# Optimization experiments

Measured on AMD Instinct MI355X. Metric: run time of the kernel, lower is better.

The kernel has to match this reference:

```python
import jax, jax.numpy as jnp
import numpy as np

B, S, IN, HID = 16, 4096, 512, 512
NH = 4
HD = HID // NH            # 128
NA = 4 * 2                # num_attractors*2 = 8 codes per head
EPS = 1e-5


def _ln(x, g, b):
    m = jnp.mean(x, axis=-1, keepdims=True)
    v = jnp.mean((x - m) ** 2, axis=-1, keepdims=True)
    return (x - m) * jax.lax.rsqrt(v + EPS) * g + b


def setup_inputs() -> dict:
    key = jax.random.key(0)
    ks = jax.random.split(key, 16)
    d = {
        "x": jax.random.normal(ks[0], (B, S, IN), jnp.float32),
        "norm_g": jnp.ones((IN,), jnp.float32),
        "norm_b": jnp.zeros((IN,), jnp.float32),
        # per-head MLP (stacked over head axis h)
        "hW1": jax.random.normal(ks[1], (NH, IN, 2 * HD), jnp.float32) / np.sqrt(IN).astype(np.float32),
        "hb1": jnp.zeros((NH, 2 * HD), jnp.float32),
        "hln_g": jnp.ones((NH, 2 * HD), jnp.float32),
        "hln_b": jnp.zeros((NH, 2 * HD), jnp.float32),
        "hW2": jax.random.normal(ks[2], (NH, 2 * HD, HD), jnp.float32) / np.sqrt(2 * HD).astype(np.float32),
        "hb2": jnp.zeros((NH, HD), jnp.float32),
        # attractor codebooks, dynamics, gates
        "attractors": jax.random.normal(ks[3], (NH, NA, HD), jnp.float32) / np.sqrt(HD).astype(np.float32),
        "dynamics": jnp.eye(HD, dtype=jnp.float32)[None] + 0.05 * jax.random.normal(ks[4], (NH, HD, HD), jnp.float32),
        "gW": jax.random.normal(ks[5], (NH, IN), jnp.float32) / np.sqrt(IN).astype(np.float32),
        "gb": jnp.zeros((NH,), jnp.float32),
        # output MLP
        "oW1": jax.random.normal(ks[6], (HID, HID), jnp.float32) / np.sqrt(HID).astype(np.float32),
        "ob1": jnp.zeros((HID,), jnp.float32),
        "oln_g": jnp.ones((HID,), jnp.float32),
        "oln_b": jnp.zeros((HID,), jnp.float32),
        "oW2": jax.random.normal(ks[7], (HID, IN), jnp.float32) / np.sqrt(HID).astype(np.float32),
        "ob2": jnp.zeros((IN,), jnp.float32),
    }
    return d


def reference(x, norm_g, norm_b, hW1, hb1, hln_g, hln_b, hW2, hb2,
              attractors, dynamics, gW, gb, oW1, ob1, oln_g, oln_b, oW2, ob2):
    xn = _ln(x, norm_g, norm_b)
    # per-head MLP (dropout is identity in eval): [B,S,NH,2HD] -> [B,S,NH,HD]
    h = jnp.einsum("bsi,hio->bsho", xn, hW1) + hb1
    h = jax.nn.gelu(_ln(h, hln_g, hln_b), approximate=False)
    state = jnp.einsum("bsho,hod->bshd", h, hW2) + hb2
    # cdist to tiny codebook via ||s||^2 + ||a||^2 - 2 s.a (matches torch.cdist matmul mode)
    s2 = jnp.sum(state * state, axis=-1, keepdims=True)          # [B,S,NH,1]
    a2 = jnp.sum(attractors * attractors, axis=-1)               # [NH,NA]
    sa = jnp.einsum("bshd,had->bsha", state, attractors)         # [B,S,NH,NA]
    dists = jnp.sqrt(jnp.maximum(s2 + a2 - 2.0 * sa, 0.0))
    attn = jax.nn.softmax(-dists / np.sqrt(HD).astype(np.float32), axis=-1)
    attr_infl = jnp.einsum("bsha,had->bshd", attn, attractors)
    dyn = jnp.einsum("bshd,hde->bshe", state, dynamics)
    gate = jax.nn.sigmoid(jnp.einsum("bsi,hi->bsh", xn, gW) + gb)[..., None]
    head_out = state + gate * 0.1 * (attr_infl - state + jnp.tanh(dyn))
    combined = head_out.reshape(*head_out.shape[:2], HID)        # concat heads
    o = combined @ oW1 + ob1
    o = jax.nn.gelu(_ln(o, oln_g, oln_b), approximate=False)
    o = o @ oW2 + ob2
    return xn + o
```

## Files before the change

kernel.cpp:

```cpp
#include <hip/hip_runtime.h>

typedef unsigned short u16;
typedef __bf16 bf16x8 __attribute__((ext_vector_type(8)));
typedef short  s16x8  __attribute__((ext_vector_type(8)));
typedef float  f32x4  __attribute__((ext_vector_type(4)));

template <bool B, class T, class F> struct cond_t { using type = T; };
template <class T, class F> struct cond_t<false, T, F> { using type = F; };
template <typename T>
__device__ auto probe_mfma(int)
    -> decltype(__builtin_amdgcn_mfma_f32_16x16x32_bf16(T{}, T{}, f32x4{}, 0, 0, 0), (char)0);
template <typename T> __device__ short probe_mfma(...);
using frag_t = typename cond_t<sizeof(probe_mfma<bf16x8>(0)) == 1, bf16x8, s16x8>::type;
#define MFMA(a, b, c) __builtin_amdgcn_mfma_f32_16x16x32_bf16((a), (b), (c), 0, 0, 0)

__device__ __forceinline__ float bf2f(u16 u) {
  unsigned int x = ((unsigned int)u) << 16; float f; __builtin_memcpy(&f, &x, 4); return f;
}
__device__ __forceinline__ u16 f2bf(float f) {
  unsigned int x; __builtin_memcpy(&x, &f, 4);
  x += 0x7fffu + ((x >> 16) & 1u);
  return (u16)(x >> 16);
}
__device__ __forceinline__ float fast_rcp(float x) { return __builtin_amdgcn_rcpf(x); }
__device__ __forceinline__ float tanh_fast(float x) {
  float t = __expf(2.0f * x);
  return 1.0f - 2.0f * fast_rcp(1.0f + t);
}
__device__ __forceinline__ float gelu_f(float x) {
  float x3 = x * x * x;
  return 0.5f * x * (1.0f + tanh_fast(0.7978845608028654f * x + 0.035677408136300125f * x3));
}
__device__ __forceinline__ float sigmoid_fast(float x) {
  return fast_rcp(1.0f + __expf(-x));
}

typedef const __attribute__((address_space(1))) void gvoid_t;
typedef __attribute__((address_space(3))) void lvoid_t;
__device__ __forceinline__ void gl16(const u16* g, char* l) {
  __builtin_amdgcn_global_load_lds((gvoid_t*)g, (lvoid_t*)l, 16, 0, 0);
}

__global__ __launch_bounds__(256) void k_tr(const float* __restrict__ src, u16* __restrict__ dst,
                                            int batch, int K, int N) {
  long KN = (long)K * N;
  long total = (long)batch * KN;
  for (long i = (long)blockIdx.x * blockDim.x + threadIdx.x; i < total;
       i += (long)gridDim.x * blockDim.x) {
    long b = i / KN; long rem = i - b * KN;
    long n = rem / K; long k = rem - n * K;
    dst[i] = f2bf(src[b * KN + k * N + n]);
  }
}

__global__ __launch_bounds__(256) void k1_ln_gate(
    const float* __restrict__ x, const float* __restrict__ ng, const float* __restrict__ nb,
    const float* __restrict__ gW, const float* __restrict__ gb,
    u16* __restrict__ xn, float* __restrict__ gate) {
  const int lane = threadIdx.x & 63;
  const long t = (long)blockIdx.x * 4 + (threadIdx.x >> 6);
  float4 a0 = *(const float4*)(x + t * 512 + lane * 8);
  float4 a1 = *(const float4*)(x + t * 512 + lane * 8 + 4);
  float f[8] = {a0.x, a0.y, a0.z, a0.w, a1.x, a1.y, a1.z, a1.w};
  float s = 0.f, ss = 0.f;
#pragma unroll
  for (int j = 0; j < 8; j++) { s += f[j]; ss += f[j] * f[j]; }
#pragma unroll
  for (int m = 1; m < 64; m <<= 1) { s += __shfl_xor(s, m); ss += __shfl_xor(ss, m); }
  const float mean = s * (1.0f / 512.0f);
  const float rstd = rsqrtf(ss * (1.0f / 512.0f) - mean * mean + 1e-5f);
  float xf[8];
  union { uint4 q; u16 u[8]; } st;
#pragma unroll
  for (int j = 0; j < 8; j++) {
    xf[j] = (f[j] - mean) * rstd * ng[lane * 8 + j] + nb[lane * 8 + j];
    st.u[j] = f2bf(xf[j]);
  }
  *(uint4*)(xn + t * 512 + lane * 8) = st.q;
  for (int h = 0; h < 4; h++) {
    float p = 0.f;
#pragma unroll
    for (int j = 0; j < 8; j++) p += xf[j] * gW[h * 512 + lane * 8 + j];
#pragma unroll
    for (int m = 1; m < 64; m <<= 1) p += __shfl_xor(p, m);
    if (lane == 0) gate[t * 4 + h] = sigmoid_fast(p + gb[h]);
  }
}

__global__ __launch_bounds__(256, 4) void k2_head(
    const u16* __restrict__ xn, const u16* __restrict__ hW1t, const float* __restrict__ hb1,
    const float* __restrict__ hlng, const float* __restrict__ hlnb,
    const u16* __restrict__ hW2t, const float* __restrict__ hb2,
    const float* __restrict__ attr, const u16* __restrict__ dynT,
    const float* __restrict__ gate, u16* __restrict__ outC) {
  __shared__ __align__(16) char smem[40960];
  const int tid = threadIdx.x;
  const int lane = tid & 63, wv = tid >> 6, q = lane >> 4, l15 = lane & 15;
  const int wr = wv >> 1, wc = wv & 1;
  const int h = blockIdx.y;
  const long t0 = (long)blockIdx.x * 64;
  const f32x4 vz = {0.f, 0.f, 0.f, 0.f};

  const int pr = lane >> 3, posp = lane & 7;
  const int pos = posp ^ pr;
  const int rl = pr * 2 + (pos >> 2), ck = pos & 3;
  const u16* gA = xn + ((size_t)(t0 + wv * 16 + rl) << 9) + ck * 8;
  const u16* gB = hW1t + ((((size_t)h * 256) + wv * 64 + rl) << 9) + ck * 8;
  char* const lA = smem + wv * 1024;
  char* const lB = smem + 8192 + wv * 4096;

  int afo[2], bfo[8];
#pragma unroll
  for (int i = 0; i < 2; i++) {
    int row = wr * 32 + i * 16 + l15;
    afo[i] = (row >> 1) * 128 + (((((row & 1) << 2) | q) ^ ((row >> 1) & 7)) << 4);
  }
#pragma unroll
  for (int nt = 0; nt < 8; nt++) {
    int row = wc * 128 + nt * 16 + l15;
    bfo[nt] = (row >> 1) * 128 + (((((row & 1) << 2) | q) ^ ((row >> 1) & 7)) << 4);
  }

  f32x4 acc[2][8];
#pragma unroll
  for (int i = 0; i < 2; i++)
#pragma unroll
    for (int nt = 0; nt < 8; nt++) acc[i][nt] = vz;

#define STAGE1(buf)                                     \
  {                                                     \
    gl16(gA, lA + (buf) * 4096);                        \
    gl16(gB, lB + (buf) * 16384);                       \
    gl16(gB + 8192, lB + (buf) * 16384 + 1024);         \
    gl16(gB + 16384, lB + (buf) * 16384 + 2048);        \
    gl16(gB + 24576, lB + (buf) * 16384 + 3072);        \
    gA += 32; gB += 32;                                 \
  }

  STAGE1(0);
  __syncthreads();
#pragma unroll 2
  for (int k = 0; k < 16; ++k) {
    const int cur = k & 1;
    if (k < 15) STAGE1(cur ^ 1);
    const char* Ab = smem + cur * 4096;
    const char* Bb = smem + 8192 + cur * 16384;
    frag_t a0 = *(const frag_t*)(Ab + afo[0]);
    frag_t a1 = *(const frag_t*)(Ab + afo[1]);
#pragma unroll
    for (int nt = 0; nt < 8; nt++) {
      frag_t bf = *(const frag_t*)(Bb + bfo[nt]);
      acc[0][nt] = MFMA(a0, bf, acc[0][nt]);
      acc[1][nt] = MFMA(a1, bf, acc[1][nt]);
    }
    __syncthreads();
  }
#undef STAGE1

  float bb[8], cg[8], cbv[8];
#pragma unroll
  for (int nt = 0; nt < 8; nt++) {
    int c = h * 256 + wc * 128 + nt * 16 + l15;
    bb[nt] = hb1[c]; cg[nt] = hlng[c]; cbv[nt] = hlnb[c];
  }
  float* sLN = (float*)(smem + 32768);
#pragma unroll
  for (int i = 0; i < 2; i++)
#pragma unroll
    for (int r = 0; r < 4; r++) {
      float s = 0.f, ss = 0.f;
#pragma unroll
      for (int nt = 0; nt < 8; nt++) { float v = acc[i][nt][r] + bb[nt]; s += v; ss = fmaf(v, v, ss); }
#pragma unroll
      for (int m = 1; m < 16; m <<= 1) { s += __shfl_xor(s, m); ss += __shfl_xor(ss, m); }
      if (l15 == 0) {
        int row = wr * 32 + i * 16 + q * 4 + r;
        sLN[row * 4 + wc * 2] = s; sLN[row * 4 + wc * 2 + 1] = ss;
      }
    }
  float* sA2 = (float*)(smem + 37888);
  if (wv == 0) {
    int a = lane >> 3, jj = lane & 7;
    float s = 0.f;
#pragma unroll
    for (int d2 = 0; d2 < 16; d2++) { float v = attr[h * 1024 + a * 128 + jj * 16 + d2]; s = fmaf(v, v, s); }
#pragma unroll
    for (int m = 1; m < 8; m <<= 1) s += __shfl_xor(s, m);
    if (jj == 0) sA2[a] = s;
  }
#pragma unroll
  for (int j = 0; j < 8; j++) {
    int idx = tid * 8 + j, ar = idx >> 7, d = idx & 127;
    u16 v = (ar < 8) ? f2bf(attr[h * 1024 + ar * 128 + d]) : (u16)0;
    *(u16*)(smem + 33792 + ar * 256 + ((2 * d) ^ ((ar & 7) << 4))) = v;
  }
  __syncthreads();
#pragma unroll
  for (int i = 0; i < 2; i++)
#pragma unroll
    for (int r = 0; r < 4; r++) {
      int row = wr * 32 + i * 16 + q * 4 + r;
      float s = sLN[row * 4] + sLN[row * 4 + 2], ss = sLN[row * 4 + 1] + sLN[row * 4 + 3];
      float mean = s * (1.f / 256.f);
      float rstd = rsqrtf(ss * (1.f / 256.f) - mean * mean + 1e-5f);
      float mr = -mean * rstd;
#pragma unroll
      for (int nt = 0; nt < 8; nt++) {
        float v = fmaf(acc[i][nt][r] + bb[nt], rstd, mr);
        v = fmaf(v, cg[nt], cbv[nt]);
        int col = wc * 128 + nt * 16 + l15;
        *(u16*)(smem + row * 512 + ((2 * col) ^ ((row & 7) << 4))) = f2bf(gelu_f(v));
      }
    }
  __syncthreads();

  f32x4 acc2[8];
#pragma unroll
  for (int nt = 0; nt < 8; nt++) acc2[nt] = vz;
  {
    const int rb2 = (wv * 16 + l15) * 512, sw2 = (l15 & 7) << 4;
    const u16* pB2[8];
#pragma unroll
    for (int nt = 0; nt < 8; nt++)
      pB2[nt] = hW2t + ((((size_t)h * 128) + nt * 16 + l15) << 8) + q * 8;
#pragma unroll
    for (int kb = 0; kb < 256; kb += 32) {
      frag_t af = *(const frag_t*)(smem + rb2 + ((kb * 2 + q * 16) ^ sw2));
#pragma unroll
      for (int nt = 0; nt < 8; nt++) {
        frag_t bf = *(const frag_t*)(pB2[nt] + kb);
        acc2[nt] = MFMA(af, bf, acc2[nt]);
      }
    }
  }
#pragma unroll
  for (int nt = 0; nt < 8; nt++) {
    float b2 = hb2[h * 128 + nt * 16 + l15];
#pragma unroll
    for (int r = 0; r < 4; r++) acc2[nt][r] += b2;
  }
  float s2v[4];
#pragma unroll
  for (int r = 0; r < 4; r++) {
    float s = 0.f;
#pragma unroll
    for (int nt = 0; nt < 8; nt++) s = fmaf(acc2[nt][r], acc2[nt][r], s);
#pragma unroll
    for (int m = 1; m < 16; m <<= 1) s += __shfl_xor(s, m);
    s2v[r] = s;
  }
  __syncthreads();

#pragma unroll
  for (int nt = 0; nt < 8; nt++)
#pragma unroll
    for (int r = 0; r < 4; r++) {
      int row = wv * 16 + q * 4 + r, col = nt * 16 + l15;
      *(u16*)(smem + row * 256 + ((2 * col) ^ ((row & 7) << 4))) = f2bf(acc2[nt][r]);
    }
#pragma unroll
  for (int j = 0; j < 16; j++) {
    int idx = tid * 16 + j, row = idx >> 5, kk = idx & 31;
    u16 v = (kk < 8) ? f2bf(attr[h * 1024 + kk * 128 + row]) : (u16)0;
    *(u16*)(smem + 20480 + row * 64 + ((2 * kk) ^ ((row & 3) << 4))) = v;
  }
  __syncthreads();

  f32x4 dacc[8], sacc = vz;
#pragma unroll
  for (int nt = 0; nt < 8; nt++) dacc[nt] = vz;
  {
    const int rb3 = (wv * 16 + l15) * 256, sw3 = (l15 & 7) << 4;
    const u16* pD[8];
#pragma unroll
    for (int nt = 0; nt < 8; nt++)
      pD[nt] = dynT + ((((size_t)h * 128) + nt * 16 + l15) << 7) + q * 8;
#pragma unroll
    for (int kb = 0; kb < 128; kb += 32) {
      const int ko = (kb * 2 + q * 16) ^ sw3;
      frag_t af = *(const frag_t*)(smem + rb3 + ko);
      frag_t ab = *(const frag_t*)(smem + 33792 + l15 * 256 + ko);
      sacc = MFMA(af, ab, sacc);
#pragma unroll
      for (int nt = 0; nt < 8; nt++) {
        frag_t bf = *(const frag_t*)(pD[nt] + kb);
        dacc[nt] = MFMA(af, bf, dacc[nt]);
      }
    }
  }

  const float dscale = 0.088388347648318447f;
  float g01[4];
#pragma unroll
  for (int r = 0; r < 4; r++)
    g01[r] = gate[(t0 + wv * 16 + q * 4 + r) * 4 + h] * 0.1f;
  const float a2l = (l15 < 8) ? ((const float*)(smem + 37888))[l15] : 0.f;
#pragma unroll
  for (int r = 0; r < 4; r++) {
    float lg = -3.0e38f;
    if (l15 < 8) {
      float d2 = fmaxf(fmaf(-2.f, sacc[r], s2v[r] + a2l), 0.f);
      lg = -sqrtf(d2) * dscale;
    }
    float mx = lg;
#pragma unroll
    for (int m = 1; m < 16; m <<= 1) mx = fmaxf(mx, __shfl_xor(mx, m));
    float p = __expf(lg - mx), den = p;
#pragma unroll
    for (int m = 1; m < 16; m <<= 1) den += __shfl_xor(den, m);
    p *= fast_rcp(den);
    int row = wv * 16 + q * 4 + r;
    *(u16*)(smem + 16384 + row * 64 + ((2 * l15) ^ ((row & 3) << 4))) = f2bf(p);
  }

#pragma unroll
  for (int nt = 0; nt < 8; nt++)
#pragma unroll
    for (int r = 0; r < 4; r++)
      dacc[nt][r] = acc2[nt][r] + g01[r] * (tanh_fast(dacc[nt][r]) - acc2[nt][r]);

  f32x4 aacc[8];
#pragma unroll
  for (int nt = 0; nt < 8; nt++) aacc[nt] = vz;
  {
    const int rowa = wv * 16 + l15;
    frag_t ap = *(const frag_t*)(smem + 16384 + rowa * 64 + ((q * 16) ^ ((l15 & 3) << 4)));
#pragma unroll
    for (int nt = 0; nt < 8; nt++) {
      int rowb = nt * 16 + l15;
      frag_t bf = *(const frag_t*)(smem + 20480 + rowb * 64 + ((q * 16) ^ ((l15 & 3) << 4)));
      aacc[nt] = MFMA(ap, bf, aacc[nt]);
    }
  }

#pragma unroll
  for (int r = 0; r < 4; r++) {
    const long t = t0 + wv * 16 + q * 4 + r;
#pragma unroll
    for (int nt = 0; nt < 8; nt++) {
      int col = nt * 16 + l15;
      outC[t * 1024 + h * 128 + col] = f2bf(dacc[nt][r] + g01[r] * aacc[nt][r]);
    }
  }
}

__global__ __launch_bounds__(256, 1) void k3_mlp1(
    const u16* __restrict__ inp, const u16* __restrict__ oW1t,
    const float* __restrict__ ob1, const float* __restrict__ olng, const float* __restrict__ olnb,
    u16* __restrict__ outp) {
  __shared__ __align__(16) char smem[46080];
  u16* sA = (u16*)smem;
  u16* sB = (u16*)(smem + 5120);
  const int tid = threadIdx.x, lane = tid & 63, wv = tid >> 6, q = lane >> 4, l15 = lane & 15;
  const long t0 = (long)blockIdx.x * 64;
  const f32x4 vz = {0.f, 0.f, 0.f, 0.f};
  f32x4 acc[32];
#pragma unroll
  for (int i = 0; i < 32; i++) acc[i] = vz;
  const int arow = tid >> 2, ako = (tid & 3) * 8;
  for (int kb = 0; kb < 512; kb += 32) {
    *(uint4*)&sA[arow * 40 + ako] = *(const uint4*)&inp[(t0 + arow) * 1024 + kb + ako];
#pragma unroll
    for (int i = 0; i < 8; i++) {
      int c = tid + 256 * i, r = c >> 2, ko = (c & 3) * 8;
      *(uint4*)&sB[r * 40 + ko] = *(const uint4*)&oW1t[(long)r * 512 + kb + ko];
    }
    __syncthreads();
    frag_t af = *(const frag_t*)&sA[(wv * 16 + l15) * 40 + q * 8];
#pragma unroll
    for (int nt = 0; nt < 32; nt++) {
      frag_t bf = *(const frag_t*)&sB[(nt * 16 + l15) * 40 + q * 8];
      acc[nt] = MFMA(af, bf, acc[nt]);
    }
    __syncthreads();
  }
  float bb[32];
#pragma unroll
  for (int nt = 0; nt < 32; nt++) bb[nt] = ob1[nt * 16 + l15];
#pragma unroll
  for (int r = 0; r < 4; r++) {
    float s = 0.f, ss = 0.f;
#pragma unroll
    for (int nt = 0; nt < 32; nt++) { float v = acc[nt][r] + bb[nt]; s += v; ss += v * v; }
#pragma unroll
    for (int m = 1; m < 16; m <<= 1) { s += __shfl_xor(s, m); ss += __shfl_xor(ss, m); }
    float mean = s * (1.f / 512.f);
    float rstd = rsqrtf(ss * (1.f / 512.f) - mean * mean + 1e-5f);
    const long t = t0 + wv * 16 + q * 4 + r;
#pragma unroll
    for (int nt = 0; nt < 32; nt++) {
      int col = nt * 16 + l15;
      float v = (acc[nt][r] + bb[nt] - mean) * rstd * olng[col] + olnb[col];
      outp[t * 1024 + col] = f2bf(gelu_f(v));
    }
  }
}

__global__ __launch_bounds__(256, 1) void k4_mlp2(
    const u16* __restrict__ inp, const u16* __restrict__ oW2t,
    const float* __restrict__ ob2, const u16* __restrict__ xn,
    float* __restrict__ outp) {
  __shared__ __align__(16) char smem[46080];
  u16* sA = (u16*)smem;
  u16* sB = (u16*)(smem + 5120);
  const int tid = threadIdx.x, lane = tid & 63, wv = tid >> 6, q = lane >> 4, l15 = lane & 15;
  const long t0 = (long)blockIdx.x * 64;
  const f32x4 vz = {0.f, 0.f, 0.f, 0.f};
  f32x4 acc[32];
#pragma unroll
  for (int i = 0; i < 32; i++) acc[i] = vz;
  const int arow = tid >> 2, ako = (tid & 3) * 8;
  for (int kb = 0; kb < 512; kb += 32) {
    *(uint4*)&sA[arow * 40 + ako] = *(const uint4*)&inp[(t0 + arow) * 1024 + kb + ako];
#pragma unroll
    for (int i = 0; i < 8; i++) {
      int c = tid + 256 * i, r = c >> 2, ko = (c & 3) * 8;
      *(uint4*)&sB[r * 40 + ko] = *(const uint4*)&oW2t[(long)r * 512 + kb + ko];
    }
    __syncthreads();
    frag_t af = *(const frag_t*)&sA[(wv * 16 + l15) * 40 + q * 8];
#pragma unroll
    for (int nt = 0; nt < 32; nt++) {
      frag_t bf = *(const frag_t*)&sB[(nt * 16 + l15) * 40 + q * 8];
      acc[nt] = MFMA(af, bf, acc[nt]);
    }
    __syncthreads();
  }
#pragma unroll
  for (int r = 0; r < 4; r++) {
    const long t = t0 + wv * 16 + q * 4 + r;
#pragma unroll
    for (int nt = 0; nt < 32; nt++) {
      int col = nt * 16 + l15;
      float v = acc[nt][r] + ob2[col] + bf2f(xn[t * 512 + col]);
      outp[t * 512 + col] = v;
    }
  }
}

extern "C" void kernel_launch(void* const* d_in, const int* in_sizes, int n_in,
                              void* d_out, int out_size, void* d_ws, size_t ws_size,
                              hipStream_t stream) {
  const float* x    = (const float*)d_in[0];
  const float* ng   = (const float*)d_in[1];
  const float* nbp  = (const float*)d_in[2];
  const float* hW1  = (const float*)d_in[3];
  const float* hb1  = (const float*)d_in[4];
  const float* hlng = (const float*)d_in[5];
  const float* hlnb = (const float*)d_in[6];
  const float* hW2  = (const float*)d_in[7];
  const float* hb2  = (const float*)d_in[8];
  const float* attr = (const float*)d_in[9];
  const float* dyn  = (const float*)d_in[10];
  const float* gW   = (const float*)d_in[11];
  const float* gb   = (const float*)d_in[12];
  const float* oW1  = (const float*)d_in[13];
  const float* ob1  = (const float*)d_in[14];
  const float* olng = (const float*)d_in[15];
  const float* olnb = (const float*)d_in[16];
  const float* oW2  = (const float*)d_in[17];
  const float* ob2  = (const float*)d_in[18];

  char* ws = (char*)d_ws;
  u16*   xn   = (u16*)ws;
  float* gate = (float*)(ws + 67108864);
  u16*   wT   = (u16*)(ws + 68157440);
  u16* hW1t = wT;
  u16* hW2t = wT + 524288;
  u16* dynT = wT + 655360;
  u16* oW1t = wT + 720896;
  u16* oW2t = wT + 983040;

  k_tr<<<512, 256, 0, stream>>>(hW1, hW1t, 4, 512, 256);
  k_tr<<<128, 256, 0, stream>>>(hW2, hW2t, 4, 256, 128);
  k_tr<<<64, 256, 0, stream>>>(dyn, dynT, 4, 128, 128);
  k_tr<<<256, 256, 0, stream>>>(oW1, oW1t, 1, 512, 512);
  k_tr<<<256, 256, 0, stream>>>(oW2, oW2t, 1, 512, 512);

  k1_ln_gate<<<16384, 256, 0, stream>>>(x, ng, nbp, gW, gb, xn, gate);

  u16* cb = (u16*)d_out;
  k2_head<<<dim3(1024, 4), 256, 0, stream>>>(xn, hW1t, hb1, hlng, hlnb, hW2t, hb2,
                                             attr, dynT, gate, cb);
  k3_mlp1<<<1024, 256, 0, stream>>>(cb, oW1t, ob1, olng, olnb, cb + 512);
  k4_mlp2<<<1024, 256, 0, stream>>>(cb + 512, oW2t, ob2, xn, (float*)d_out);
}
```

Before: 838.2 us.

## Restructure GEMM staging across head, MLP1 and MLP2 kernels

The head kernel's first GEMM drops LDS double-buffering and reads A and B fragments straight from global memory. Its output is now staged through swizzled LDS so it can be written back as coalesced 16-byte stores. MLP1 and MLP2 are re-tiled: each wave owns 128 output columns and all 64 rows. The weight tile is double-buffered in LDS through async global-to-LDS loads while A fragments are read directly from global memory, and launch bounds rise to 2 blocks per CU. MLP1's LayerNorm now reduces across waves through shared memory, and the direct global reads in the head GEMM risk losing reuse.

```diff
diff --git a/kernel.cpp b/kernel.cpp
--- a/kernel.cpp
+++ b/kernel.cpp
@@ -101,61 +101,30 @@
   const long t0 = (long)blockIdx.x * 64;
   const f32x4 vz = {0.f, 0.f, 0.f, 0.f};
 
-  const int pr = lane >> 3, posp = lane & 7;
-  const int pos = posp ^ pr;
-  const int rl = pr * 2 + (pos >> 2), ck = pos & 3;
-  const u16* gA = xn + ((size_t)(t0 + wv * 16 + rl) << 9) + ck * 8;
-  const u16* gB = hW1t + ((((size_t)h * 256) + wv * 64 + rl) << 9) + ck * 8;
-  char* const lA = smem + wv * 1024;
-  char* const lB = smem + 8192 + wv * 4096;
-
-  int afo[2], bfo[8];
-#pragma unroll
-  for (int i = 0; i < 2; i++) {
-    int row = wr * 32 + i * 16 + l15;
-    afo[i] = (row >> 1) * 128 + (((((row & 1) << 2) | q) ^ ((row >> 1) & 7)) << 4);
-  }
-#pragma unroll
-  for (int nt = 0; nt < 8; nt++) {
-    int row = wc * 128 + nt * 16 + l15;
-    bfo[nt] = (row >> 1) * 128 + (((((row & 1) << 2) | q) ^ ((row >> 1) & 7)) << 4);
-  }
-
   f32x4 acc[2][8];
 #pragma unroll
   for (int i = 0; i < 2; i++)
 #pragma unroll
     for (int nt = 0; nt < 8; nt++) acc[i][nt] = vz;
-
-#define STAGE1(buf)                                     \
-  {                                                     \
-    gl16(gA, lA + (buf) * 4096);                        \
-    gl16(gB, lB + (buf) * 16384);                       \
-    gl16(gB + 8192, lB + (buf) * 16384 + 1024);         \
-    gl16(gB + 16384, lB + (buf) * 16384 + 2048);        \
-    gl16(gB + 24576, lB + (buf) * 16384 + 3072);        \
-    gA += 32; gB += 32;                                 \
-  }
-
-  STAGE1(0);
-  __syncthreads();
+  {
+    const u16* pA0 = xn + (((size_t)(t0 + wr * 32 + l15)) << 9) + q * 8;
+    const u16* pA1 = pA0 + (16 << 9);
+    const u16* pB1[8];
+#pragma unroll
+    for (int nt = 0; nt < 8; nt++)
+      pB1[nt] = hW1t + (((size_t)h * 256 + wc * 128 + nt * 16 + l15) << 9) + q * 8;
 #pragma unroll 2
-  for (int k = 0; k < 16; ++k) {
-    const int cur = k & 1;
-    if (k < 15) STAGE1(cur ^ 1);
-    const char* Ab = smem + cur * 4096;
-    const char* Bb = smem + 8192 + cur * 16384;
-    frag_t a0 = *(const frag_t*)(Ab + afo[0]);
-    frag_t a1 = *(const frag_t*)(Ab + afo[1]);
-#pragma unroll
-    for (int nt = 0; nt < 8; nt++) {
-      frag_t bf = *(const frag_t*)(Bb + bfo[nt]);
-      acc[0][nt] = MFMA(a0, bf, acc[0][nt]);
-      acc[1][nt] = MFMA(a1, bf, acc[1][nt]);
-    }
-    __syncthreads();
-  }
-#undef STAGE1
+    for (int kb = 0; kb < 512; kb += 32) {
+      frag_t a0 = *(const frag_t*)(pA0 + kb);
+      frag_t a1 = *(const frag_t*)(pA1 + kb);
+#pragma unroll
+      for (int nt = 0; nt < 8; nt++) {
+        frag_t bf = *(const frag_t*)(pB1[nt] + kb);
+        acc[0][nt] = MFMA(a0, bf, acc[0][nt]);
+        acc[1][nt] = MFMA(a1, bf, acc[1][nt]);
+      }
+    }
+  }
 
   float bb[8], cg[8], cbv[8];
 #pragma unroll
@@ -335,107 +304,185 @@
 
 #pragma unroll
   for (int r = 0; r < 4; r++) {
-    const long t = t0 + wv * 16 + q * 4 + r;
+    int row = wv * 16 + q * 4 + r;
+    int key = (row >> 2) & 3;
 #pragma unroll
     for (int nt = 0; nt < 8; nt++) {
       int col = nt * 16 + l15;
-      outC[t * 1024 + h * 128 + col] = f2bf(dacc[nt][r] + g01[r] * aacc[nt][r]);
-    }
-  }
-}
-
-__global__ __launch_bounds__(256, 1) void k3_mlp1(
+      float ho = dacc[nt][r] + g01[r] * aacc[nt][r];
+      *(u16*)(smem + row * 256 + ((2 * col) ^ (key << 5))) = f2bf(ho);
+    }
+  }
+  {
+    const int row = tid >> 2;
+    const int key = (row >> 2) & 3;
+    const long t = t0 + row;
+#pragma unroll
+    for (int j = 0; j < 4; j++) {
+      int c = (tid & 3) + 4 * j;
+      uint4 v = *(const uint4*)(smem + row * 256 + ((c << 4) ^ (key << 5)));
+      *(uint4*)(outC + t * 1024 + h * 128 + c * 8) = v;
+    }
+  }
+}
+
+__global__ __launch_bounds__(256, 2) void k3_mlp1(
     const u16* __restrict__ inp, const u16* __restrict__ oW1t,
     const float* __restrict__ ob1, const float* __restrict__ olng, const float* __restrict__ olnb,
     u16* __restrict__ outp) {
-  __shared__ __align__(16) char smem[46080];
-  u16* sA = (u16*)smem;
-  u16* sB = (u16*)(smem + 5120);
+  __shared__ __align__(16) char smem[67584];
   const int tid = threadIdx.x, lane = tid & 63, wv = tid >> 6, q = lane >> 4, l15 = lane & 15;
   const long t0 = (long)blockIdx.x * 64;
   const f32x4 vz = {0.f, 0.f, 0.f, 0.f};
-  f32x4 acc[32];
-#pragma unroll
-  for (int i = 0; i < 32; i++) acc[i] = vz;
-  const int arow = tid >> 2, ako = (tid & 3) * 8;
-  for (int kb = 0; kb < 512; kb += 32) {
-    *(uint4*)&sA[arow * 40 + ako] = *(const uint4*)&inp[(t0 + arow) * 1024 + kb + ako];
-#pragma unroll
-    for (int i = 0; i < 8; i++) {
-      int c = tid + 256 * i, r = c >> 2, ko = (c & 3) * 8;
-      *(uint4*)&sB[r * 40 + ko] = *(const uint4*)&oW1t[(long)r * 512 + kb + ko];
+  f32x4 acc[4][8];
+#pragma unroll
+  for (int i = 0; i < 4; i++)
+#pragma unroll
+    for (int nt = 0; nt < 8; nt++) acc[i][nt] = vz;
+
+  const int pr = lane >> 3, pos = (lane & 7) ^ pr;
+  const int rl = pr * 2 + (pos >> 2), ck = pos & 3;
+  const u16* gB = oW1t + ((size_t)(wv * 128 + rl) << 9) + ck * 8;
+  int bfo[8];
+#pragma unroll
+  for (int nt = 0; nt < 8; nt++) {
+    int row = wv * 128 + nt * 16 + l15;
+    bfo[nt] = (row >> 1) * 128 + (((((row & 1) << 2) | q) ^ ((row >> 1) & 7)) << 4);
+  }
+  const u16* pA = inp + (((size_t)(t0 + l15)) << 10) + q * 8;
+
+#define STG3(buf, kb)                                                      \
+  {                                                                        \
+    char* l = smem + (buf) * 32768 + wv * 8192;                            \
+    _Pragma("unroll") for (int m = 0; m < 8; m++)                          \
+        gl16(gB + m * 8192 + (kb), l + m * 1024);                          \
+  }
+
+  STG3(0, 0);
+  __syncthreads();
+  for (int k = 0; k < 16; ++k) {
+    const int kb = k * 32, cur = k & 1;
+    frag_t a[4];
+#pragma unroll
+    for (int i = 0; i < 4; i++) a[i] = *(const frag_t*)(pA + i * 16384 + kb);
+    if (k < 15) STG3(cur ^ 1, kb + 32);
+    const char* Bb = smem + cur * 32768;
+#pragma unroll
+    for (int nt = 0; nt < 8; nt++) {
+      frag_t bf = *(const frag_t*)(Bb + bfo[nt]);
+#pragma unroll
+      for (int i = 0; i < 4; i++) acc[i][nt] = MFMA(a[i], bf, acc[i][nt]);
     }
     __syncthreads();
-    frag_t af = *(const frag_t*)&sA[(wv * 16 + l15) * 40 + q * 8];
-#pragma unroll
-    for (int nt = 0; nt < 32; nt++) {
-      frag_t bf = *(const frag_t*)&sB[(nt * 16 + l15) * 40 + q * 8];
-      acc[nt] = MFMA(af, bf, acc[nt]);
-    }
-    __syncthreads();
-  }
-  float bb[32];
-#pragma unroll
-  for (int nt = 0; nt < 32; nt++) bb[nt] = ob1[nt * 16 + l15];
-#pragma unroll
-  for (int r = 0; r < 4; r++) {
-    float s = 0.f, ss = 0.f;
-#pragma unroll
-    for (int nt = 0; nt < 32; nt++) { float v = acc[nt][r] + bb[nt]; s += v; ss += v * v; }
-#pragma unroll
-    for (int m = 1; m < 16; m <<= 1) { s += __shfl_xor(s, m); ss += __shfl_xor(ss, m); }
-    float mean = s * (1.f / 512.f);
-    float rstd = rsqrtf(ss * (1.f / 512.f) - mean * mean + 1e-5f);
-    const long t = t0 + wv * 16 + q * 4 + r;
-#pragma unroll
-    for (int nt = 0; nt < 32; nt++) {
-      int col = nt * 16 + l15;
-      float v = (acc[nt][r] + bb[nt] - mean) * rstd * olng[col] + olnb[col];
-      outp[t * 1024 + col] = f2bf(gelu_f(v));
-    }
-  }
-}
-
-__global__ __launch_bounds__(256, 1) void k4_mlp2(
+  }
+#undef STG3
+
+  float bb[8], cg[8], cb2[8];
+#pragma unroll
+  for (int nt = 0; nt < 8; nt++) {
+    int col = wv * 128 + nt * 16 + l15;
+    bb[nt] = ob1[col]; cg[nt] = olng[col]; cb2[nt] = olnb[col];
+  }
+  float* sLN = (float*)(smem + 65536);
+#pragma unroll
+  for (int i = 0; i < 4; i++)
+#pragma unroll
+    for (int r = 0; r < 4; r++) {
+      float s = 0.f, ss = 0.f;
+#pragma unroll
+      for (int nt = 0; nt < 8; nt++) { float v = acc[i][nt][r] + bb[nt]; s += v; ss = fmaf(v, v, ss); }
+#pragma unroll
+      for (int m = 1; m < 16; m <<= 1) { s += __shfl_xor(s, m); ss += __shfl_xor(ss, m); }
+      if (l15 == 0) {
+        int row = i * 16 + q * 4 + r;
+        sLN[row * 8 + wv * 2] = s; sLN[row * 8 + wv * 2 + 1] = ss;
+      }
+    }
+  __syncthreads();
+#pragma unroll
+  for (int i = 0; i < 4; i++)
+#pragma unroll
+    for (int r = 0; r < 4; r++) {
+      int row = i * 16 + q * 4 + r;
+      float4 p0 = *(const float4*)&sLN[row * 8];
+      float4 p1 = *(const float4*)&sLN[row * 8 + 4];
+      float s = p0.x + p0.z + p1.x + p1.z, ss = p0.y + p0.w + p1.y + p1.w;
+      float mean = s * (1.f / 512.f);
+      float rstd = rsqrtf(ss * (1.f / 512.f) - mean * mean + 1e-5f);
+      const long t = t0 + row;
+#pragma unroll
+      for (int nt = 0; nt < 8; nt++) {
+        int col = wv * 128 + nt * 16 + l15;
+        float v = (acc[i][nt][r] + bb[nt] - mean) * rstd * cg[nt] + cb2[nt];
+        outp[t * 1024 + col] = f2bf(gelu_f(v));
+      }
+    }
+}
+
+__global__ __launch_bounds__(256, 2) void k4_mlp2(
     const u16* __restrict__ inp, const u16* __restrict__ oW2t,
     const float* __restrict__ ob2, const u16* __restrict__ xn,
     float* __restrict__ outp) {
-  __shared__ __align__(16) char smem[46080];
-  u16* sA = (u16*)smem;
-  u16* sB = (u16*)(smem + 5120);
+  __shared__ __align__(16) char smem[65536];
   const int tid = threadIdx.x, lane = tid & 63, wv = tid >> 6, q = lane >> 4, l15 = lane & 15;
   const long t0 = (long)blockIdx.x * 64;
   const f32x4 vz = {0.f, 0.f, 0.f, 0.f};
-  f32x4 acc[32];
-#pragma unroll
-  for (int i = 0; i < 32; i++) acc[i] = vz;
-  const int arow = tid >> 2, ako = (tid & 3) * 8;
-  for (int kb = 0; kb < 512; kb += 32) {
-    *(uint4*)&sA[arow * 40 + ako] = *(const uint4*)&inp[(t0 + arow) * 1024 + kb + ako];
-#pragma unroll
-    for (int i = 0; i < 8; i++) {
-      int c = tid + 256 * i, r = c >> 2, ko = (c & 3) * 8;
-      *(uint4*)&sB[r * 40 + ko] = *(const uint4*)&oW2t[(long)r * 512 + kb + ko];
+  f32x4 acc[4][8];
+#pragma unroll
+  for (int i = 0; i < 4; i++)
+#pragma unroll
+    for (int nt = 0; nt < 8; nt++) acc[i][nt] = vz;
+
+  const int pr = lane >> 3, pos = (lane & 7) ^ pr;
+  const int rl = pr * 2 + (pos >> 2), ck = pos & 3;
+  const u16* gB = oW2t + ((size_t)(wv * 128 + rl) << 9) + ck * 8;
+  int bfo[8];
+#pragma unroll
+  for (int nt = 0; nt < 8; nt++) {
+    int row = wv * 128 + nt * 16 + l15;
+    bfo[nt] = (row >> 1) * 128 + (((((row & 1) << 2) | q) ^ ((row >> 1) & 7)) << 4);
+  }
+  const u16* pA = inp + (((size_t)(t0 + l15)) << 10) + q * 8;
+
+#define STG4(buf, kb)                                                      \
+  {                                                                        \
+    char* l = smem + (buf) * 32768 + wv * 8192;                            \
+    _Pragma("unroll") for (int m = 0; m < 8; m++)                          \
+        gl16(gB + m * 8192 + (kb), l + m * 1024);                          \
+  }
+
+  STG4(0, 0);
+  __syncthreads();
+  for (int k = 0; k < 16; ++k) {
+    const int kb = k * 32, cur = k & 1;
+    frag_t a[4];
+#pragma unroll
+    for (int i = 0; i < 4; i++) a[i] = *(const frag_t*)(pA + i * 16384 + kb);
+    if (k < 15) STG4(cur ^ 1, kb + 32);
+    const char* Bb = smem + cur * 32768;
+#pragma unroll
+    for (int nt = 0; nt < 8; nt++) {
+      frag_t bf = *(const frag_t*)(Bb + bfo[nt]);
+#pragma unroll
+      for (int i = 0; i < 4; i++) acc[i][nt] = MFMA(a[i], bf, acc[i][nt]);
     }
     __syncthreads();
-    frag_t af = *(const frag_t*)&sA[(wv * 16 + l15) * 40 + q * 8];
-#pragma unroll
-    for (int nt = 0; nt < 32; nt++) {
-      frag_t bf = *(const frag_t*)&sB[(nt * 16 + l15) * 40 + q * 8];
-      acc[nt] = MFMA(af, bf, acc[nt]);
-    }
-    __syncthreads();
-  }
-#pragma unroll
-  for (int r = 0; r < 4; r++) {
-    const long t = t0 + wv * 16 + q * 4 + r;
-#pragma unroll
-    for (int nt = 0; nt < 32; nt++) {
-      int col = nt * 16 + l15;
-      float v = acc[nt][r] + ob2[col] + bf2f(xn[t * 512 + col]);
-      outp[t * 512 + col] = v;
-    }
-  }
+  }
+#undef STG4
+
+#pragma unroll
+  for (int i = 0; i < 4; i++)
+#pragma unroll
+    for (int r = 0; r < 4; r++) {
+      int row = i * 16 + q * 4 + r;
+      const long t = t0 + row;
+#pragma unroll
+      for (int nt = 0; nt < 8; nt++) {
+        int col = wv * 128 + nt * 16 + l15;
+        float v = acc[i][nt][r] + ob2[col] + bf2f(xn[t * 512 + col]);
+        outp[t * 512 + col] = v;
+      }
+    }
 }
 
 extern "C" void kernel_launch(void* const* d_in, const int* in_sizes, int n_in,
```

After: 1.013 ms. +20.8%, slower.
